# Optimization experiments

Measured on AMD Instinct MI355X. Metric: run time of the kernel, lower is better.

## Reference

```python
import jax, jax.numpy as jnp
import numpy as np

B, C, H, W = 4, 192, 128, 128
NH = 6
HD = C // NH            # 32
GS = 8                  # window (group) size
K = 16                  # unfold kernel size
STRIDE, PAD = 8, 4
NUM = H // GS           # 16 groups per side
BG = B * NUM * NUM      # 1024 windows
N = GS * GS             # 64 tokens per group
KK = K * K              # 256 sampled tokens per window
SCALE = HD ** -0.5


def _rope(x):
    # lucidrains-style rotary embedding along dim -2 (positions), last dim = head_dim
    d = x.shape[-1]
    inv = 1.0 / (10000.0 ** (jnp.arange(0, d, 2, dtype=jnp.float32) / d))
    t = jnp.arange(x.shape[-2], dtype=jnp.float32)
    freqs = jnp.repeat(t[:, None] * inv[None, :], 2, axis=-1)  # [seq, d], interleaved
    cos, sin = jnp.cos(freqs), jnp.sin(freqs)
    xp = x.reshape(x.shape[:-1] + (d // 2, 2))
    xr = jnp.stack((-xp[..., 1], xp[..., 0]), axis=-1).reshape(x.shape)
    return x * cos + xr * sin


def _l2norm(x):
    # torch F.normalize(dim=-1): x / max(||x||, eps)
    n = jnp.linalg.norm(x, axis=-1, keepdims=True)
    return x / jnp.maximum(n, 1e-12)


def setup_inputs() -> dict:
    key = jax.random.key(0)
    ks = jax.random.split(key, 6)
    return {
        "x_complete": jax.random.normal(ks[0], (B, C, H, W), jnp.float32),
        "graph": jax.random.randint(ks[1], (BG, 1, N, KK), 0, 2) > 0,
        "w_group": jax.random.normal(ks[2], (C, C), jnp.float32) * 0.02,
        "b_group": jnp.zeros((C,), jnp.float32),
        "w_sample": jax.random.normal(ks[3], (2 * C, C), jnp.float32) * 0.02,
        "b_sample": jnp.zeros((2 * C,), jnp.float32),
        "w_proj": jax.random.normal(ks[4], (C, C), jnp.float32) * 0.02,
        "b_proj": jnp.zeros((C,), jnp.float32),
    }


def reference(x_complete, graph, w_group, b_group, w_sample, b_sample, w_proj, b_proj):
    # --- local grouping: [B,C,(numh sh),(numw sw)] -> [(B numh numw), sh*sw, C]
    xg = x_complete.reshape(B, C, NUM, GS, NUM, GS).transpose(0, 2, 4, 3, 5, 1).reshape(BG, N, C)
    # --- proj_group: 1x1 Conv1d over channels, then split heads 'b (h c) n -> b h n c'
    x1 = jnp.einsum('bnc,dc->bnd', xg, w_group) + b_group
    x1 = x1.reshape(BG, N, NH, HD).transpose(0, 2, 1, 3)            # [BG,NH,N,HD]
    # --- proj_sample: 1x1 Conv2d to 2C channels
    xs = jnp.einsum('bchw,dc->bdhw', x_complete, w_sample) + b_sample[None, :, None, None]
    # --- F.unfold(kernel=16, stride=8, pad=4): patch features channel-major (c,k0,k1)
    patches = jax.lax.conv_general_dilated_patches(
        xs, (K, K), (STRIDE, STRIDE), ((PAD, PAD), (PAD, PAD)))    # [B, 2C*KK, NUM, NUM]
    xs = patches.reshape(B, 2 * C, KK, NUM * NUM).transpose(0, 3, 2, 1).reshape(BG, KK, 2 * C)
    # --- 'b n (div h c) -> div b h n c'
    xs = xs.reshape(BG, KK, 2, NH, HD)
    x2 = xs[:, :, 0].transpose(0, 2, 1, 3)                          # [BG,NH,KK,HD]
    feat = xs[:, :, 1].transpose(0, 2, 1, 3)                        # [BG,NH,KK,HD]
    # --- RoPE + masked cosine-sim attention
    q = _rope(x1)
    k = _rope(x2)
    sim = jnp.einsum('bhmc,bhnc->bhmn', _l2norm(q), _l2norm(k))
    sim = sim + (-100.0) * (~graph).astype(sim.dtype)
    corr = jax.nn.softmax(sim * SCALE, axis=-1)                     # [BG,NH,N,KK]
    out = jnp.einsum('bhmn,bhnc->bhmc', corr, feat)                 # [BG,NH,N,HD]
    out = out.transpose(0, 2, 1, 3).reshape(BG, N, C)
    return out @ w_proj.T + b_proj
```

## Files before the change

### kernel.cpp

```cpp
#include <hip/hip_runtime.h>
#include <hip/hip_bf16.h>

#define B_    4
#define C_    192
#define C2_   384
#define PIX_  16384
#define NH_   6
#define BG_   1024
#define SCALE_ 0.17677669529663687f
#define C1_ 0.2550348943f

typedef __attribute__((ext_vector_type(8))) short short8v;
typedef __attribute__((ext_vector_type(4))) float f32x4;

__device__ __forceinline__ unsigned cvt_pk_bf16(float lo, float hi) {
    unsigned r;
    asm("v_cvt_pk_bf16_f32 %0, %1, %2" : "=v"(r) : "v"(lo), "v"(hi));
    return r;
}

__global__ __launch_bounds__(256, 1)
void k_rope_init(float2* __restrict__ tbl) {
    int e = blockIdx.x * 256 + threadIdx.x;
    if (e >= 4096) return;
    int pos = e >> 4, j = e & 15;
    float freq = powf(10.0f, -0.25f * (float)j);
    float ang = (float)pos * freq;
    float sn, cs;
    sincosf(ang, &sn, &cs);
    tbl[e] = make_float2(cs, sn);
}

__global__ __launch_bounds__(256, 4)
void k_gmask(const int* __restrict__ g, unsigned int* __restrict__ gbits) {
    int e = blockIdx.x * 256 + threadIdx.x;
    const uint4* p = (const uint4*)(g + (size_t)e * 32);
    unsigned int m = 0u;
#pragma unroll
    for (int i = 0; i < 8; ++i) {
        uint4 v = p[i];
        m |= (v.x ? 1u : 0u) << (i * 4);
        m |= (v.y ? 1u : 0u) << (i * 4 + 1);
        m |= (v.z ? 1u : 0u) << (i * 4 + 2);
        m |= (v.w ? 1u : 0u) << (i * 4 + 3);
    }
    gbits[e] = m;
}

__global__ __launch_bounds__(256, 4)
void k_wcast(const float* __restrict__ wsm, const float* __restrict__ wgb,
             const float* __restrict__ wpj, __hip_bfloat16* __restrict__ wb)
{
    int e = (blockIdx.x * 256 + threadIdx.x) * 4;
    float4 v = (e < 73728) ? *(const float4*)(wsm + e)
             : (e < 110592) ? *(const float4*)(wgb + (e - 73728))
                            : *(const float4*)(wpj + (e - 110592));
    uint2 pk = make_uint2(cvt_pk_bf16(v.x, v.y), cvt_pk_bf16(v.z, v.w));
    *(uint2*)(wb + e) = pk;
}

__global__ __launch_bounds__(256, 4)
void k_convm(const float* __restrict__ x, const __hip_bfloat16* __restrict__ wb,
             const float* __restrict__ bsm, const float* __restrict__ bgb,
             const float2* __restrict__ tbl,
             __hip_bfloat16* __restrict__ xsk, __hip_bfloat16* __restrict__ xsv,
             __hip_bfloat16* __restrict__ qbf)
{
    __shared__ __align__(16) char smem[25600];
    const int bid = blockIdx.x;
    const int b = bid >> 8, pt = bid & 255;
    const int px0 = pt * 64;
    const int t = threadIdx.x;

    {
        const int px = t & 63, cq = t >> 6;
        const float* src = x + ((size_t)b * C_ + cq * 48) * PIX_ + px0 + px;
        char* row = smem + px * 400 + cq * 96;
#pragma unroll
        for (int i = 0; i < 6; ++i) {
            float f[8];
#pragma unroll
            for (int j = 0; j < 8; ++j) f[j] = src[(size_t)(i * 8 + j) * PIX_];
            uint4 pk4;
            pk4.x = cvt_pk_bf16(f[0], f[1]); pk4.y = cvt_pk_bf16(f[2], f[3]);
            pk4.z = cvt_pk_bf16(f[4], f[5]); pk4.w = cvt_pk_bf16(f[6], f[7]);
            *(uint4*)(row + i * 16) = pk4;
        }
    }
    __syncthreads();

    const int w = t >> 6, lane = t & 63;
    const int l15 = lane & 15, g = lane >> 4;
    const int mb = (w & 1) * 32;
    const int nb = (w >> 1) * 32;

    short8v xf0[6], xf1[6];
#pragma unroll
    for (int ks = 0; ks < 6; ++ks) {
        xf0[ks] = *(const short8v*)(smem + (mb + l15) * 400      + ks * 64 + g * 16);
        xf1[ks] = *(const short8v*)(smem + (mb + 16 + l15) * 400 + ks * 64 + g * 16);
    }

    const f32x4 zz = {0.0f, 0.0f, 0.0f, 0.0f};

#pragma unroll
    for (int o2 = 0; o2 < 3; ++o2) {
        const int oct = 3 + o2;
        f32x4 acc00 = zz, acc01 = zz, acc10 = zz, acc11 = zz;
        const __hip_bfloat16* w0 = wb + (size_t)(oct * 64 + nb + l15) * C_;
        const __hip_bfloat16* w1 = w0 + 16 * C_;
#pragma unroll
        for (int ks = 0; ks < 6; ++ks) {
            const short8v b0 = *(const short8v*)(w0 + ks * 32 + g * 8);
            const short8v b1 = *(const short8v*)(w1 + ks * 32 + g * 8);
            acc00 = __builtin_amdgcn_mfma_f32_16x16x32_bf16(xf0[ks], b0, acc00, 0, 0, 0);
            acc01 = __builtin_amdgcn_mfma_f32_16x16x32_bf16(xf0[ks], b1, acc01, 0, 0, 0);
            acc10 = __builtin_amdgcn_mfma_f32_16x16x32_bf16(xf1[ks], b0, acc10, 0, 0, 0);
            acc11 = __builtin_amdgcn_mfma_f32_16x16x32_bf16(xf1[ks], b1, acc11, 0, 0, 0);
        }
        const float bo0 = bsm[oct * 64 + nb + l15];
        const float bo1 = bsm[oct * 64 + nb + 16 + l15];
        uint2 p00 = make_uint2(cvt_pk_bf16(acc00[0] + bo0, acc00[1] + bo0),
                               cvt_pk_bf16(acc00[2] + bo0, acc00[3] + bo0));
        uint2 p10 = make_uint2(cvt_pk_bf16(acc10[0] + bo0, acc10[1] + bo0),
                               cvt_pk_bf16(acc10[2] + bo0, acc10[3] + bo0));
        uint2 p01 = make_uint2(cvt_pk_bf16(acc01[0] + bo1, acc01[1] + bo1),
                               cvt_pk_bf16(acc01[2] + bo1, acc01[3] + bo1));
        uint2 p11 = make_uint2(cvt_pk_bf16(acc11[0] + bo1, acc11[1] + bo1),
                               cvt_pk_bf16(acc11[2] + bo1, acc11[3] + bo1));
        __hip_bfloat16* d0 = xsv + (size_t)(b * C_ + o2 * 64 + nb + l15) * PIX_
                                 + px0 + mb + g * 4;
        *(uint2*)d0        = p00;
        *(uint2*)(d0 + 16) = p10;
        __hip_bfloat16* d1 = d0 + (size_t)16 * PIX_;
        *(uint2*)d1        = p01;
        *(uint2*)(d1 + 16) = p11;
    }

#pragma unroll
    for (int o2 = 0; o2 < 3; ++o2) {
        const int oct = o2;
        f32x4 a00 = zz, a01 = zz, a10 = zz, a11 = zz;
        const __hip_bfloat16* w0 = wb + (size_t)(oct * 64 + nb + l15) * C_;
        const __hip_bfloat16* w1 = w0 + 16 * C_;
#pragma unroll
        for (int ks = 0; ks < 6; ++ks) {
            const short8v wf0 = *(const short8v*)(w0 + ks * 32 + g * 8);
            const short8v wf1 = *(const short8v*)(w1 + ks * 32 + g * 8);
            a00 = __builtin_amdgcn_mfma_f32_16x16x32_bf16(wf0, xf0[ks], a00, 0, 0, 0);
            a01 = __builtin_amdgcn_mfma_f32_16x16x32_bf16(wf0, xf1[ks], a01, 0, 0, 0);
            a10 = __builtin_amdgcn_mfma_f32_16x16x32_bf16(wf1, xf0[ks], a10, 0, 0, 0);
            a11 = __builtin_amdgcn_mfma_f32_16x16x32_bf16(wf1, xf1[ks], a11, 0, 0, 0);
        }
        const float4 bv0 = *(const float4*)(bsm + oct * 64 + nb + g * 4);
        const float4 bv1 = *(const float4*)(bsm + oct * 64 + nb + 16 + g * 4);
        a00[0] += bv0.x; a00[1] += bv0.y; a00[2] += bv0.z; a00[3] += bv0.w;
        a01[0] += bv0.x; a01[1] += bv0.y; a01[2] += bv0.z; a01[3] += bv0.w;
        a10[0] += bv1.x; a10[1] += bv1.y; a10[2] += bv1.z; a10[3] += bv1.w;
        a11[0] += bv1.x; a11[1] += bv1.y; a11[2] += bv1.z; a11[3] += bv1.w;
        float s0 = 0.0f, s1 = 0.0f;
#pragma unroll
        for (int j = 0; j < 4; ++j) {
            s0 = fmaf(a00[j], a00[j], s0); s0 = fmaf(a10[j], a10[j], s0);
            s1 = fmaf(a01[j], a01[j], s1); s1 = fmaf(a11[j], a11[j], s1);
        }
        s0 += __shfl_xor(s0, 16); s0 += __shfl_xor(s0, 32);
        s1 += __shfl_xor(s1, 16); s1 += __shfl_xor(s1, 32);
        const float inv0 = 1.0f / fmaxf(sqrtf(s0), 1e-12f);
        const float inv1 = 1.0f / fmaxf(sqrtf(s1), 1e-12f);
        uint2 q00 = make_uint2(cvt_pk_bf16(a00[0] * inv0, a00[1] * inv0),
                               cvt_pk_bf16(a00[2] * inv0, a00[3] * inv0));
        uint2 q10 = make_uint2(cvt_pk_bf16(a10[0] * inv0, a10[1] * inv0),
                               cvt_pk_bf16(a10[2] * inv0, a10[3] * inv0));
        uint2 q01 = make_uint2(cvt_pk_bf16(a01[0] * inv1, a01[1] * inv1),
                               cvt_pk_bf16(a01[2] * inv1, a01[3] * inv1));
        uint2 q11 = make_uint2(cvt_pk_bf16(a11[0] * inv1, a11[1] * inv1),
                               cvt_pk_bf16(a11[2] * inv1, a11[3] * inv1));
        __hip_bfloat16* d0 = xsk + ((size_t)b * PIX_ + px0 + mb + l15) * C_
                                 + oct * 64 + nb + g * 4;
        *(uint2*)d0        = q00;
        *(uint2*)(d0 + 16) = q10;
        __hip_bfloat16* d1 = d0 + (size_t)16 * C_;
        *(uint2*)d1        = q01;
        *(uint2*)(d1 + 16) = q11;
    }

    const int r = pt >> 1;
    const int c0q = (pt & 1) * 64 + mb + l15;
    const int n0 = (r & 7) * 8 + (c0q & 7);
    const int n1 = (r & 7) * 8 + ((c0q + 16) & 7);
    const int bg0 = (b << 8) + ((r >> 3) << 4) + (c0q >> 3);
    const int bg1 = (b << 8) + ((r >> 3) << 4) + ((c0q + 16) >> 3);
#pragma unroll
    for (int o2 = 0; o2 < 3; ++o2) {
        const int oct = 6 + o2;
        f32x4 a00 = zz, a01 = zz, a10 = zz, a11 = zz;
        const __hip_bfloat16* w0 = wb + (size_t)(oct * 64 + nb + l15) * C_;
        const __hip_bfloat16* w1 = w0 + 16 * C_;
#pragma unroll
        for (int ks = 0; ks < 6; ++ks) {
            const short8v wf0 = *(const short8v*)(w0 + ks * 32 + g * 8);
            const short8v wf1 = *(const short8v*)(w1 + ks * 32 + g * 8);
            a00 = __builtin_amdgcn_mfma_f32_16x16x32_bf16(wf0, xf0[ks], a00, 0, 0, 0);
            a01 = __builtin_amdgcn_mfma_f32_16x16x32_bf16(wf0, xf1[ks], a01, 0, 0, 0);
            a10 = __builtin_amdgcn_mfma_f32_16x16x32_bf16(wf1, xf0[ks], a10, 0, 0, 0);
            a11 = __builtin_amdgcn_mfma_f32_16x16x32_bf16(wf1, xf1[ks], a11, 0, 0, 0);
        }
        const float4 bv0 = *(const float4*)(bgb + (oct - 6) * 64 + nb + g * 4);
        const float4 bv1 = *(const float4*)(bgb + (oct - 6) * 64 + nb + 16 + g * 4);
        a00[0] += bv0.x; a00[1] += bv0.y; a00[2] += bv0.z; a00[3] += bv0.w;
        a01[0] += bv0.x; a01[1] += bv0.y; a01[2] += bv0.z; a01[3] += bv0.w;
        a10[0] += bv1.x; a10[1] += bv1.y; a10[2] += bv1.z; a10[3] += bv1.w;
        a11[0] += bv1.x; a11[1] += bv1.y; a11[2] += bv1.z; a11[3] += bv1.w;
        {
            float2 cA, cB;
            cA = tbl[n0 * 16 + g * 2]; cB = tbl[n0 * 16 + g * 2 + 1];
            { float u0 = a00[0], u1 = a00[1];
              a00[0] = u0 * cA.x - u1 * cA.y; a00[1] = u1 * cA.x + u0 * cA.y; }
            { float u0 = a00[2], u1 = a00[3];
              a00[2] = u0 * cB.x - u1 * cB.y; a00[3] = u1 * cB.x + u0 * cB.y; }
            cA = tbl[n0 * 16 + 8 + g * 2]; cB = tbl[n0 * 16 + 8 + g * 2 + 1];
            { float u0 = a10[0], u1 = a10[1];
              a10[0] = u0 * cA.x - u1 * cA.y; a10[1] = u1 * cA.x + u0 * cA.y; }
            { float u0 = a10[2], u1 = a10[3];
              a10[2] = u0 * cB.x - u1 * cB.y; a10[3] = u1 * cB.x + u0 * cB.y; }
            cA = tbl[n1 * 16 + g * 2]; cB = tbl[n1 * 16 + g * 2 + 1];
            { float u0 = a01[0], u1 = a01[1];
              a01[0] = u0 * cA.x - u1 * cA.y; a01[1] = u1 * cA.x + u0 * cA.y; }
            { float u0 = a01[2], u1 = a01[3];
              a01[2] = u0 * cB.x - u1 * cB.y; a01[3] = u1 * cB.x + u0 * cB.y; }
            cA = tbl[n1 * 16 + 8 + g * 2]; cB = tbl[n1 * 16 + 8 + g * 2 + 1];
            { float u0 = a11[0], u1 = a11[1];
              a11[0] = u0 * cA.x - u1 * cA.y; a11[1] = u1 * cA.x + u0 * cA.y; }
            { float u0 = a11[2], u1 = a11[3];
              a11[2] = u0 * cB.x - u1 * cB.y; a11[3] = u1 * cB.x + u0 * cB.y; }
        }
        float s0 = 0.0f, s1 = 0.0f;
#pragma unroll
        for (int j = 0; j < 4; ++j) {
            s0 = fmaf(a00[j], a00[j], s0); s0 = fmaf(a10[j], a10[j], s0);
            s1 = fmaf(a01[j], a01[j], s1); s1 = fmaf(a11[j], a11[j], s1);
        }
        s0 += __shfl_xor(s0, 16); s0 += __shfl_xor(s0, 32);
        s1 += __shfl_xor(s1, 16); s1 += __shfl_xor(s1, 32);
        const float inv0 = 1.0f / fmaxf(sqrtf(s0), 1e-12f);
        const float inv1 = 1.0f / fmaxf(sqrtf(s1), 1e-12f);
        uint2 q00 = make_uint2(cvt_pk_bf16(a00[0] * inv0, a00[1] * inv0),
                               cvt_pk_bf16(a00[2] * inv0, a00[3] * inv0));
        uint2 q10 = make_uint2(cvt_pk_bf16(a10[0] * inv0, a10[1] * inv0),
                               cvt_pk_bf16(a10[2] * inv0, a10[3] * inv0));
        uint2 q01 = make_uint2(cvt_pk_bf16(a01[0] * inv1, a01[1] * inv1),
                               cvt_pk_bf16(a01[2] * inv1, a01[3] * inv1));
        uint2 q11 = make_uint2(cvt_pk_bf16(a11[0] * inv1, a11[1] * inv1),
                               cvt_pk_bf16(a11[2] * inv1, a11[3] * inv1));
        const int hglob = (oct - 6) * 2 + (nb >> 5);
        __hip_bfloat16* d0 = qbf + (((size_t)bg0 * NH_ + hglob) * 64 + n0) * 32 + g * 4;
        *(uint2*)d0        = q00;
        *(uint2*)(d0 + 16) = q10;
        __hip_bfloat16* d1 = qbf + (((size_t)bg1 * NH_ + hglob) * 64 + n1) * 32 + g * 4;
        *(uint2*)d1        = q01;
        *(uint2*)(d1 + 16) = q11;
    }
}

__global__ __launch_bounds__(512, 2)
void k_attn(const __hip_bfloat16* __restrict__ xsk, const __hip_bfloat16* __restrict__ xsv,
            const unsigned int* __restrict__ gbits, const __hip_bfloat16* __restrict__ qb,
            const float2* __restrict__ tbl, float* __restrict__ attn)
{
    __shared__ __align__(16) char smem[52736];
    const int bid0 = blockIdx.x;
    const int bid = (bid0 & 7) * 768 + (bid0 >> 3);
    const int h = bid % NH_;
    const int bg = bid / NH_;
    const int b = bg >> 8, ph = (bg >> 4) & 15, pw = bg & 15;
    const int t = threadIdx.x;
    const int w = t >> 6, lane = t & 63;
    const int g = lane >> 4, l15 = lane & 15;
    const int rbase = (w & 3) * 16;
    const int wcol  = w >> 2;
    const int cb    = wcol * 128;
    const int cb32  = wcol * 4;

    const short8v qa = *(const short8v*)(qb +
        ((size_t)(bg * NH_ + h) * 64 + rbase + l15) * 32 + g * 8);

    {
        const int m = t >> 1, half = t & 1;
        const int k0 = m >> 4, k1 = m & 15;
        const int rr = ph * 8 - 4 + k0, cc = pw * 8 - 4 + k1;
        const bool inb = ((unsigned)rr < 128u) && ((unsigned)cc < 128u);
        float kv[16];
        if (inb) {
            const uint4* pk = (const uint4*)(xsk +
                ((size_t)b * PIX_ + rr * 128 + cc) * C_ + h * 32 + half * 16);
            union { uint4 u; __hip_bfloat16 h8[8]; } r0, r1;
            r0.u = pk[0]; r1.u = pk[1];
#pragma unroll
            for (int d = 0; d < 8; ++d) {
                kv[d]     = __bfloat162float(r0.h8[d]);
                kv[8 + d] = __bfloat162float(r1.h8[d]);
            }
        } else {
#pragma unroll
            for (int d = 0; d < 16; ++d) kv[d] = 0.0f;
        }
        unsigned pk8[8];
#pragma unroll
        for (int p = 0; p < 8; ++p) {
            float2 cs = tbl[m * 16 + half * 8 + p];
            float a0 = kv[2 * p], a1 = kv[2 * p + 1];
            float e0 = a0 * cs.x - a1 * cs.y;
            float e1 = a1 * cs.x + a0 * cs.y;
            pk8[p] = cvt_pk_bf16(e0, e1);
        }
        *(uint4*)(smem + m * 80 + half * 32)      = make_uint4(pk8[0], pk8[1], pk8[2], pk8[3]);
        *(uint4*)(smem + m * 80 + half * 32 + 16) = make_uint4(pk8[4], pk8[5], pk8[6], pk8[7]);
    }

    {
        const int d = t & 31, k0 = t >> 5;
        const int rr = ph * 8 - 4 + k0;
        const int c0 = pw * 8 - 4;
        char* dst = smem + 34816 + d * 528 + k0 * 32;
        const __hip_bfloat16* src = xsv + (size_t)(b * C_ + h * 32 + d) * PIX_ + rr * 128 + c0;
        const bool rok = (unsigned)rr < 128u;
        if (rok && pw >= 1 && pw <= 14) {
            const uint2* s2 = (const uint2*)src;
            uint2 a0 = s2[0], a1 = s2[1], a2 = s2[2], a3 = s2[3];
            ((uint4*)dst)[0] = make_uint4(a0.x, a0.y, a1.x, a1.y);
            ((uint4*)dst)[1] = make_uint4(a2.x, a2.y, a3.x, a3.y);
        } else {
            __hip_bfloat16* dh = (__hip_bfloat16*)dst;
            __hip_bfloat16 z = __float2bfloat16(0.0f);
#pragma unroll
            for (int i = 0; i < 16; ++i) {
                bool ok = rok && ((unsigned)(c0 + i) < 128u);
                dh[i] = ok ? src[i] : z;
            }
        }
    }

    {
        unsigned int* gbl = (unsigned int*)(smem + 20480);
        const int q = t >> 3, wd = t & 7;
        gbl[q * 9 + wd] = gbits[(size_t)bg * 512 + t];
    }
    __syncthreads();

    f32x4 acc[8];
    const f32x4 zz = {0.0f, 0.0f, 0.0f, 0.0f};
#pragma unroll
    for (int tile = 0; tile < 8; ++tile) {
        const short8v kb = *(const short8v*)(smem + (cb + tile * 16 + l15) * 80 + g * 16);
        acc[tile] = __builtin_amdgcn_mfma_f32_16x16x32_bf16(kb, qa, zz, 0, 0, 0);
    }

    const unsigned int* gbl = (const unsigned int*)(smem + 20480);
    float* reds = (float*)(smem + 51712);
    {
        const int q = rbase + l15;
        const unsigned int wv[4] = { gbl[q * 9 + cb32], gbl[q * 9 + cb32 + 1],
                                     gbl[q * 9 + cb32 + 2], gbl[q * 9 + cb32 + 3] };
        float sm = 0.0f;
#pragma unroll
        for (int tile = 0; tile < 8; ++tile) {
            const unsigned int bits = wv[tile >> 1] >> ((tile & 1) * 16 + (g << 2));
#pragma unroll
            for (int j = 0; j < 4; ++j) {
                float e = __builtin_amdgcn_exp2f(fmaf(acc[tile][j], C1_, -C1_));
                e = ((bits >> j) & 1u) ? e : 0.0f;
                acc[tile][j] = e;
                sm += e;
            }
        }
        sm += __shfl_xor(sm, 16);
        sm += __shfl_xor(sm, 32);
        if (lane < 16) reds[q * 2 + wcol] = sm;
    }
    __syncthreads();

    float inv4[4];
#pragma unroll
    for (int j = 0; j < 4; ++j) {
        const int qq = rbase + (g << 2) + j;
        float2 rr2 = *(const float2*)&reds[qq * 2];
        inv4[j] = 1.0f / (rr2.x + rr2.y + 1e-37f);
    }

    char* plw = smem + w * 4352;
#pragma unroll
    for (int tile = 0; tile < 8; ++tile) {
        uint2 pw2 = make_uint2(cvt_pk_bf16(acc[tile][0], acc[tile][1]),
                               cvt_pk_bf16(acc[tile][2], acc[tile][3]));
        *(uint2*)(plw + l15 * 272 + tile * 32 + g * 8) = pw2;
    }

    f32x4 o0 = zz, o1 = zz;
#pragma unroll
    for (int ks = 0; ks < 4; ++ks) {
        const short8v pa  = *(const short8v*)(plw + l15 * 272 + (ks * 32 + g * 8) * 2);
        const short8v vb0 = *(const short8v*)(smem + 34816 + l15 * 528        + (cb + ks * 32 + g * 8) * 2);
        const short8v vb1 = *(const short8v*)(smem + 34816 + (16 + l15) * 528 + (cb + ks * 32 + g * 8) * 2);
        o0 = __builtin_amdgcn_mfma_f32_16x16x32_bf16(pa, vb0, o0, 0, 0, 0);
        o1 = __builtin_amdgcn_mfma_f32_16x16x32_bf16(pa, vb1, o1, 0, 0, 0);
    }
    __syncthreads();

    float* ob = (float*)smem;
    if (wcol == 1) {
#pragma unroll
        for (int j = 0; j < 4; ++j) {
            const int q = rbase + g * 4 + j;
            ob[q * 33 + l15]      = o0[j];
            ob[q * 33 + 16 + l15] = o1[j];
        }
    }
    __syncthreads();
    if (wcol == 0) {
#pragma unroll
        for (int j = 0; j < 4; ++j) {
            const int q = rbase + g * 4 + j;
            float v0 = (o0[j] + ob[q * 33 + l15])      * inv4[j];
            float v1 = (o1[j] + ob[q * 33 + 16 + l15]) * inv4[j];
            attn[((size_t)bg * 64 + q) * 192 + h * 32 + l15]      = v0;
            attn[((size_t)bg * 64 + q) * 192 + h * 32 + 16 + l15] = v1;
        }
    }
}

__global__ __launch_bounds__(256, 4)
void k_oprojm(const float* __restrict__ attn, const __hip_bfloat16* __restrict__ wpb,
              const float* __restrict__ bp, float* __restrict__ out)
{
    __shared__ __align__(16) char smem[25600];
    const int bid0 = blockIdx.x;
    const int bid = (bid0 & 7) * 384 + (bid0 >> 3);
    const int oct = bid % 3;
    const int rt  = bid / 3;
    const int row0 = rt * 64;
    const int t = threadIdx.x;

#pragma unroll
    for (int e0 = 0; e0 < 12; ++e0) {
        const int e = e0 * 256 + t;
        const int r = e / 48, c4 = e % 48;
        float4 v = *(const float4*)(attn + (size_t)(row0 + r) * 192 + c4 * 4);
        uint2 pk = make_uint2(cvt_pk_bf16(v.x, v.y), cvt_pk_bf16(v.z, v.w));
        *(uint2*)(smem + r * 400 + c4 * 8) = pk;
    }
    __syncthreads();

    const int w = t >> 6, lane = t & 63;
    const int l15 = lane & 15, g = lane >> 4;
    const int mb = (w & 1) * 32;
    const int nb = (w >> 1) * 32;

    const f32x4 zz = {0.0f, 0.0f, 0.0f, 0.0f};
    f32x4 acc00 = zz, acc01 = zz, acc10 = zz, acc11 = zz;
    const __hip_bfloat16* w0 = wpb + (size_t)(oct * 64 + nb + l15) * C_;
    const __hip_bfloat16* w1 = w0 + 16 * C_;
#pragma unroll
    for (int ks = 0; ks < 6; ++ks) {
        const short8v a0 = *(const short8v*)(smem + (mb + l15) * 400      + ks * 64 + g * 16);
        const short8v a1 = *(const short8v*)(smem + (mb + 16 + l15) * 400 + ks * 64 + g * 16);
        const short8v b0 = *(const short8v*)(w0 + ks * 32 + g * 8);
        const short8v b1 = *(const short8v*)(w1 + ks * 32 + g * 8);
        acc00 = __builtin_amdgcn_mfma_f32_16x16x32_bf16(a0, b0, acc00, 0, 0, 0);
        acc01 = __builtin_amdgcn_mfma_f32_16x16x32_bf16(a0, b1, acc01, 0, 0, 0);
        acc10 = __builtin_amdgcn_mfma_f32_16x16x32_bf16(a1, b0, acc10, 0, 0, 0);
        acc11 = __builtin_amdgcn_mfma_f32_16x16x32_bf16(a1, b1, acc11, 0, 0, 0);
    }
    __syncthreads();

    float* ot = (float*)smem;
#pragma unroll
    for (int j = 0; j < 4; ++j) {
        ot[(mb + g * 4 + j) * 68      + nb + l15]      = acc00[j];
        ot[(mb + 16 + g * 4 + j) * 68 + nb + l15]      = acc10[j];
        ot[(mb + g * 4 + j) * 68      + nb + 16 + l15] = acc01[j];
        ot[(mb + 16 + g * 4 + j) * 68 + nb + 16 + l15] = acc11[j];
    }
    __syncthreads();

    {
        const int k = t & 15, pxi = t >> 4;
        const float4 bias4 = *(const float4*)(bp + oct * 64 + k * 4);
#pragma unroll
        for (int p = 0; p < 4; ++p) {
            const int px = p * 16 + pxi;
            float4 v = *(const float4*)&ot[px * 68 + k * 4];
            v.x += bias4.x; v.y += bias4.y; v.z += bias4.z; v.w += bias4.w;
            *(float4*)(out + (size_t)(row0 + px) * 192 + oct * 64 + k * 4) = v;
        }
    }
}

extern "C" void kernel_launch(void* const* d_in, const int* in_sizes, int n_in,
                              void* d_out, int out_size, void* d_ws, size_t ws_size,
                              hipStream_t stream)
{
    (void)in_sizes; (void)n_in; (void)out_size; (void)ws_size;
    const float* x   = (const float*)d_in[0];
    const int* grph  = (const int*)d_in[1];
    const float* wg  = (const float*)d_in[2];
    const float* bgb = (const float*)d_in[3];
    const float* wsm = (const float*)d_in[4];
    const float* bsm = (const float*)d_in[5];
    const float* wp  = (const float*)d_in[6];
    const float* bp  = (const float*)d_in[7];
    float* out = (float*)d_out;

    char* wsb = (char*)d_ws;
    __hip_bfloat16* xsk = (__hip_bfloat16*)wsb;
    __hip_bfloat16* xsv = (__hip_bfloat16*)(wsb + 25165824ull);
    __hip_bfloat16* qbf = (__hip_bfloat16*)(wsb + 50331648ull);
    float2* tbl = (float2*)(wsb + 75497472ull);
    unsigned int* gbits = (unsigned int*)(wsb + 75530240ull);
    __hip_bfloat16* wb  = (__hip_bfloat16*)(wsb + 77627392ull);
    __hip_bfloat16* wpb = wb + 110592;

    hipLaunchKernelGGL(k_rope_init, dim3(16),   dim3(256), 0, stream, tbl);
    hipLaunchKernelGGL(k_wcast,     dim3(144),  dim3(256), 0, stream, wsm, wg, wp, wb);
    hipLaunchKernelGGL(k_gmask,     dim3(2048), dim3(256), 0, stream, grph, gbits);
    hipLaunchKernelGGL(k_convm,     dim3(1024), dim3(256), 0, stream, x, wb, bsm, bgb, tbl, xsk, xsv, qbf);
    hipLaunchKernelGGL(k_attn,      dim3(6144), dim3(512), 0, stream, xsk, xsv, gbits, qbf, tbl, out);
    hipLaunchKernelGGL(k_oprojm,    dim3(3072), dim3(256), 0, stream, out, wpb, bp, out);
}
```

Before: 186.0 us.

## Halve k_convm pixel tile to 32 and double grid with XCD-aware block swizzle

The fused 1x1-conv kernel now processes 32 pixels per block instead of 64, so each wave computes a 16x32 output tile with half the accumulators and A-fragments. Shared memory per block halves, launch bounds request 8 blocks/SM, and the grid doubles to 2048 blocks. Block indices are remapped so consecutive hardware blocks land on the same XCD. This aims for more occupancy and better latency hiding, at the cost of reloading weight fragments twice as often per pixel.

```diff
diff --git a/kernel.cpp b/kernel.cpp
--- a/kernel.cpp
+++ b/kernel.cpp
@@ -59,25 +59,26 @@
     *(uint2*)(wb + e) = pk;
 }
 
-__global__ __launch_bounds__(256, 4)
+__global__ __launch_bounds__(256, 8)
 void k_convm(const float* __restrict__ x, const __hip_bfloat16* __restrict__ wb,
              const float* __restrict__ bsm, const float* __restrict__ bgb,
              const float2* __restrict__ tbl,
              __hip_bfloat16* __restrict__ xsk, __hip_bfloat16* __restrict__ xsv,
              __hip_bfloat16* __restrict__ qbf)
 {
-    __shared__ __align__(16) char smem[25600];
-    const int bid = blockIdx.x;
-    const int b = bid >> 8, pt = bid & 255;
-    const int px0 = pt * 64;
+    __shared__ __align__(16) char smem[12800];
+    const int bid0 = blockIdx.x;
+    const int bid = (bid0 & 7) * 256 + (bid0 >> 3);
+    const int b = bid >> 9, pt = bid & 511;
+    const int px0 = pt * 32;
     const int t = threadIdx.x;
 
     {
-        const int px = t & 63, cq = t >> 6;
-        const float* src = x + ((size_t)b * C_ + cq * 48) * PIX_ + px0 + px;
-        char* row = smem + px * 400 + cq * 96;
-#pragma unroll
-        for (int i = 0; i < 6; ++i) {
+        const int px = t & 31, cq = t >> 5;
+        const float* src = x + ((size_t)b * C_ + cq * 24) * PIX_ + px0 + px;
+        char* row = smem + px * 400 + cq * 48;
+#pragma unroll
+        for (int i = 0; i < 3; ++i) {
             float f[8];
 #pragma unroll
             for (int j = 0; j < 8; ++j) f[j] = src[(size_t)(i * 8 + j) * PIX_];
@@ -91,175 +92,125 @@
 
     const int w = t >> 6, lane = t & 63;
     const int l15 = lane & 15, g = lane >> 4;
-    const int mb = (w & 1) * 32;
-    const int nb = (w >> 1) * 32;
-
-    short8v xf0[6], xf1[6];
-#pragma unroll
-    for (int ks = 0; ks < 6; ++ks) {
-        xf0[ks] = *(const short8v*)(smem + (mb + l15) * 400      + ks * 64 + g * 16);
-        xf1[ks] = *(const short8v*)(smem + (mb + 16 + l15) * 400 + ks * 64 + g * 16);
-    }
+    const int pb2 = (w & 1) * 16;
+    const int ob2 = (w >> 1) * 32;
+
+    short8v xf[6];
+#pragma unroll
+    for (int ks = 0; ks < 6; ++ks)
+        xf[ks] = *(const short8v*)(smem + (pb2 + l15) * 400 + ks * 64 + g * 16);
 
     const f32x4 zz = {0.0f, 0.0f, 0.0f, 0.0f};
 
 #pragma unroll
     for (int o2 = 0; o2 < 3; ++o2) {
         const int oct = 3 + o2;
-        f32x4 acc00 = zz, acc01 = zz, acc10 = zz, acc11 = zz;
-        const __hip_bfloat16* w0 = wb + (size_t)(oct * 64 + nb + l15) * C_;
+        f32x4 acc0 = zz, acc1 = zz;
+        const __hip_bfloat16* w0 = wb + (size_t)(oct * 64 + ob2 + l15) * C_;
         const __hip_bfloat16* w1 = w0 + 16 * C_;
 #pragma unroll
         for (int ks = 0; ks < 6; ++ks) {
             const short8v b0 = *(const short8v*)(w0 + ks * 32 + g * 8);
             const short8v b1 = *(const short8v*)(w1 + ks * 32 + g * 8);
-            acc00 = __builtin_amdgcn_mfma_f32_16x16x32_bf16(xf0[ks], b0, acc00, 0, 0, 0);
-            acc01 = __builtin_amdgcn_mfma_f32_16x16x32_bf16(xf0[ks], b1, acc01, 0, 0, 0);
-            acc10 = __builtin_amdgcn_mfma_f32_16x16x32_bf16(xf1[ks], b0, acc10, 0, 0, 0);
-            acc11 = __builtin_amdgcn_mfma_f32_16x16x32_bf16(xf1[ks], b1, acc11, 0, 0, 0);
-        }
-        const float bo0 = bsm[oct * 64 + nb + l15];
-        const float bo1 = bsm[oct * 64 + nb + 16 + l15];
-        uint2 p00 = make_uint2(cvt_pk_bf16(acc00[0] + bo0, acc00[1] + bo0),
-                               cvt_pk_bf16(acc00[2] + bo0, acc00[3] + bo0));
-        uint2 p10 = make_uint2(cvt_pk_bf16(acc10[0] + bo0, acc10[1] + bo0),
-                               cvt_pk_bf16(acc10[2] + bo0, acc10[3] + bo0));
-        uint2 p01 = make_uint2(cvt_pk_bf16(acc01[0] + bo1, acc01[1] + bo1),
-                               cvt_pk_bf16(acc01[2] + bo1, acc01[3] + bo1));
-        uint2 p11 = make_uint2(cvt_pk_bf16(acc11[0] + bo1, acc11[1] + bo1),
-                               cvt_pk_bf16(acc11[2] + bo1, acc11[3] + bo1));
-        __hip_bfloat16* d0 = xsv + (size_t)(b * C_ + o2 * 64 + nb + l15) * PIX_
-                                 + px0 + mb + g * 4;
-        *(uint2*)d0        = p00;
-        *(uint2*)(d0 + 16) = p10;
-        __hip_bfloat16* d1 = d0 + (size_t)16 * PIX_;
-        *(uint2*)d1        = p01;
-        *(uint2*)(d1 + 16) = p11;
+            acc0 = __builtin_amdgcn_mfma_f32_16x16x32_bf16(xf[ks], b0, acc0, 0, 0, 0);
+            acc1 = __builtin_amdgcn_mfma_f32_16x16x32_bf16(xf[ks], b1, acc1, 0, 0, 0);
+        }
+        const float bo0 = bsm[oct * 64 + ob2 + l15];
+        const float bo1 = bsm[oct * 64 + ob2 + 16 + l15];
+        uint2 p0 = make_uint2(cvt_pk_bf16(acc0[0] + bo0, acc0[1] + bo0),
+                              cvt_pk_bf16(acc0[2] + bo0, acc0[3] + bo0));
+        uint2 p1 = make_uint2(cvt_pk_bf16(acc1[0] + bo1, acc1[1] + bo1),
+                              cvt_pk_bf16(acc1[2] + bo1, acc1[3] + bo1));
+        __hip_bfloat16* d0 = xsv + (size_t)(b * C_ + o2 * 64 + ob2 + l15) * PIX_
+                                 + px0 + pb2 + g * 4;
+        *(uint2*)d0 = p0;
+        *(uint2*)(d0 + (size_t)16 * PIX_) = p1;
     }
 
 #pragma unroll
     for (int o2 = 0; o2 < 3; ++o2) {
         const int oct = o2;
-        f32x4 a00 = zz, a01 = zz, a10 = zz, a11 = zz;
-        const __hip_bfloat16* w0 = wb + (size_t)(oct * 64 + nb + l15) * C_;
+        f32x4 a0 = zz, a1 = zz;
+        const __hip_bfloat16* w0 = wb + (size_t)(oct * 64 + ob2 + l15) * C_;
         const __hip_bfloat16* w1 = w0 + 16 * C_;
 #pragma unroll
         for (int ks = 0; ks < 6; ++ks) {
             const short8v wf0 = *(const short8v*)(w0 + ks * 32 + g * 8);
             const short8v wf1 = *(const short8v*)(w1 + ks * 32 + g * 8);
-            a00 = __builtin_amdgcn_mfma_f32_16x16x32_bf16(wf0, xf0[ks], a00, 0, 0, 0);
-            a01 = __builtin_amdgcn_mfma_f32_16x16x32_bf16(wf0, xf1[ks], a01, 0, 0, 0);
-            a10 = __builtin_amdgcn_mfma_f32_16x16x32_bf16(wf1, xf0[ks], a10, 0, 0, 0);
-            a11 = __builtin_amdgcn_mfma_f32_16x16x32_bf16(wf1, xf1[ks], a11, 0, 0, 0);
-        }
-        const float4 bv0 = *(const float4*)(bsm + oct * 64 + nb + g * 4);
-        const float4 bv1 = *(const float4*)(bsm + oct * 64 + nb + 16 + g * 4);
-        a00[0] += bv0.x; a00[1] += bv0.y; a00[2] += bv0.z; a00[3] += bv0.w;
-        a01[0] += bv0.x; a01[1] += bv0.y; a01[2] += bv0.z; a01[3] += bv0.w;
-        a10[0] += bv1.x; a10[1] += bv1.y; a10[2] += bv1.z; a10[3] += bv1.w;
-        a11[0] += bv1.x; a11[1] += bv1.y; a11[2] += bv1.z; a11[3] += bv1.w;
-        float s0 = 0.0f, s1 = 0.0f;
+            a0 = __builtin_amdgcn_mfma_f32_16x16x32_bf16(wf0, xf[ks], a0, 0, 0, 0);
+            a1 = __builtin_amdgcn_mfma_f32_16x16x32_bf16(wf1, xf[ks], a1, 0, 0, 0);
+        }
+        const float4 bv0 = *(const float4*)(bsm + oct * 64 + ob2 + g * 4);
+        const float4 bv1 = *(const float4*)(bsm + oct * 64 + ob2 + 16 + g * 4);
+        a0[0] += bv0.x; a0[1] += bv0.y; a0[2] += bv0.z; a0[3] += bv0.w;
+        a1[0] += bv1.x; a1[1] += bv1.y; a1[2] += bv1.z; a1[3] += bv1.w;
+        float s = 0.0f;
 #pragma unroll
         for (int j = 0; j < 4; ++j) {
-            s0 = fmaf(a00[j], a00[j], s0); s0 = fmaf(a10[j], a10[j], s0);
-            s1 = fmaf(a01[j], a01[j], s1); s1 = fmaf(a11[j], a11[j], s1);
-        }
-        s0 += __shfl_xor(s0, 16); s0 += __shfl_xor(s0, 32);
-        s1 += __shfl_xor(s1, 16); s1 += __shfl_xor(s1, 32);
-        const float inv0 = 1.0f / fmaxf(sqrtf(s0), 1e-12f);
-        const float inv1 = 1.0f / fmaxf(sqrtf(s1), 1e-12f);
-        uint2 q00 = make_uint2(cvt_pk_bf16(a00[0] * inv0, a00[1] * inv0),
-                               cvt_pk_bf16(a00[2] * inv0, a00[3] * inv0));
-        uint2 q10 = make_uint2(cvt_pk_bf16(a10[0] * inv0, a10[1] * inv0),
-                               cvt_pk_bf16(a10[2] * inv0, a10[3] * inv0));
-        uint2 q01 = make_uint2(cvt_pk_bf16(a01[0] * inv1, a01[1] * inv1),
-                               cvt_pk_bf16(a01[2] * inv1, a01[3] * inv1));
-        uint2 q11 = make_uint2(cvt_pk_bf16(a11[0] * inv1, a11[1] * inv1),
-                               cvt_pk_bf16(a11[2] * inv1, a11[3] * inv1));
-        __hip_bfloat16* d0 = xsk + ((size_t)b * PIX_ + px0 + mb + l15) * C_
-                                 + oct * 64 + nb + g * 4;
-        *(uint2*)d0        = q00;
-        *(uint2*)(d0 + 16) = q10;
-        __hip_bfloat16* d1 = d0 + (size_t)16 * C_;
-        *(uint2*)d1        = q01;
-        *(uint2*)(d1 + 16) = q11;
-    }
-
-    const int r = pt >> 1;
-    const int c0q = (pt & 1) * 64 + mb + l15;
-    const int n0 = (r & 7) * 8 + (c0q & 7);
-    const int n1 = (r & 7) * 8 + ((c0q + 16) & 7);
-    const int bg0 = (b << 8) + ((r >> 3) << 4) + (c0q >> 3);
-    const int bg1 = (b << 8) + ((r >> 3) << 4) + ((c0q + 16) >> 3);
+            s = fmaf(a0[j], a0[j], s);
+            s = fmaf(a1[j], a1[j], s);
+        }
+        s += __shfl_xor(s, 16); s += __shfl_xor(s, 32);
+        const float inv = 1.0f / fmaxf(sqrtf(s), 1e-12f);
+        uint2 q0 = make_uint2(cvt_pk_bf16(a0[0] * inv, a0[1] * inv),
+                              cvt_pk_bf16(a0[2] * inv, a0[3] * inv));
+        uint2 q1 = make_uint2(cvt_pk_bf16(a1[0] * inv, a1[1] * inv),
+                              cvt_pk_bf16(a1[2] * inv, a1[3] * inv));
+        __hip_bfloat16* d = xsk + ((size_t)b * PIX_ + px0 + pb2 + l15) * C_
+                                + oct * 64 + ob2 + g * 4;
+        *(uint2*)d        = q0;
+        *(uint2*)(d + 16) = q1;
+    }
+
+    const int p  = px0 + pb2 + l15;
+    const int r  = p >> 7, c = p & 127;
+    const int n  = (r & 7) * 8 + (c & 7);
+    const int bg = (b << 8) + ((r >> 3) << 4) + (c >> 3);
 #pragma unroll
     for (int o2 = 0; o2 < 3; ++o2) {
         const int oct = 6 + o2;
-        f32x4 a00 = zz, a01 = zz, a10 = zz, a11 = zz;
-        const __hip_bfloat16* w0 = wb + (size_t)(oct * 64 + nb + l15) * C_;
+        f32x4 a0 = zz, a1 = zz;
+        const __hip_bfloat16* w0 = wb + (size_t)(oct * 64 + ob2 + l15) * C_;
         const __hip_bfloat16* w1 = w0 + 16 * C_;
 #pragma unroll
         for (int ks = 0; ks < 6; ++ks) {
             const short8v wf0 = *(const short8v*)(w0 + ks * 32 + g * 8);
             const short8v wf1 = *(const short8v*)(w1 + ks * 32 + g * 8);
-            a00 = __builtin_amdgcn_mfma_f32_16x16x32_bf16(wf0, xf0[ks], a00, 0, 0, 0);
-            a01 = __builtin_amdgcn_mfma_f32_16x16x32_bf16(wf0, xf1[ks], a01, 0, 0, 0);
-            a10 = __builtin_amdgcn_mfma_f32_16x16x32_bf16(wf1, xf0[ks], a10, 0, 0, 0);
-            a11 = __builtin_amdgcn_mfma_f32_16x16x32_bf16(wf1, xf1[ks], a11, 0, 0, 0);
-        }
-        const float4 bv0 = *(const float4*)(bgb + (oct - 6) * 64 + nb + g * 4);
-        const float4 bv1 = *(const float4*)(bgb + (oct - 6) * 64 + nb + 16 + g * 4);
-        a00[0] += bv0.x; a00[1] += bv0.y; a00[2] += bv0.z; a00[3] += bv0.w;
-        a01[0] += bv0.x; a01[1] += bv0.y; a01[2] += bv0.z; a01[3] += bv0.w;
-        a10[0] += bv1.x; a10[1] += bv1.y; a10[2] += bv1.z; a10[3] += bv1.w;
-        a11[0] += bv1.x; a11[1] += bv1.y; a11[2] += bv1.z; a11[3] += bv1.w;
+            a0 = __builtin_amdgcn_mfma_f32_16x16x32_bf16(wf0, xf[ks], a0, 0, 0, 0);
+            a1 = __builtin_amdgcn_mfma_f32_16x16x32_bf16(wf1, xf[ks], a1, 0, 0, 0);
+        }
+        const float4 bv0 = *(const float4*)(bgb + (oct - 6) * 64 + ob2 + g * 4);
+        const float4 bv1 = *(const float4*)(bgb + (oct - 6) * 64 + ob2 + 16 + g * 4);
+        a0[0] += bv0.x; a0[1] += bv0.y; a0[2] += bv0.z; a0[3] += bv0.w;
+        a1[0] += bv1.x; a1[1] += bv1.y; a1[2] += bv1.z; a1[3] += bv1.w;
         {
-            float2 cA, cB;
-            cA = tbl[n0 * 16 + g * 2]; cB = tbl[n0 * 16 + g * 2 + 1];
-            { float u0 = a00[0], u1 = a00[1];
-              a00[0] = u0 * cA.x - u1 * cA.y; a00[1] = u1 * cA.x + u0 * cA.y; }
-            { float u0 = a00[2], u1 = a00[3];
-              a00[2] = u0 * cB.x - u1 * cB.y; a00[3] = u1 * cB.x + u0 * cB.y; }
-            cA = tbl[n0 * 16 + 8 + g * 2]; cB = tbl[n0 * 16 + 8 + g * 2 + 1];
-            { float u0 = a10[0], u1 = a10[1];
-              a10[0] = u0 * cA.x - u1 * cA.y; a10[1] = u1 * cA.x + u0 * cA.y; }
-            { float u0 = a10[2], u1 = a10[3];
-              a10[2] = u0 * cB.x - u1 * cB.y; a10[3] = u1 * cB.x + u0 * cB.y; }
-            cA = tbl[n1 * 16 + g * 2]; cB = tbl[n1 * 16 + g * 2 + 1];
-            { float u0 = a01[0], u1 = a01[1];
-              a01[0] = u0 * cA.x - u1 * cA.y; a01[1] = u1 * cA.x + u0 * cA.y; }
-            { float u0 = a01[2], u1 = a01[3];
-              a01[2] = u0 * cB.x - u1 * cB.y; a01[3] = u1 * cB.x + u0 * cB.y; }
-            cA = tbl[n1 * 16 + 8 + g * 2]; cB = tbl[n1 * 16 + 8 + g * 2 + 1];
-            { float u0 = a11[0], u1 = a11[1];
-              a11[0] = u0 * cA.x - u1 * cA.y; a11[1] = u1 * cA.x + u0 * cA.y; }
-            { float u0 = a11[2], u1 = a11[3];
-              a11[2] = u0 * cB.x - u1 * cB.y; a11[3] = u1 * cB.x + u0 * cB.y; }
-        }
-        float s0 = 0.0f, s1 = 0.0f;
+            float2 cA = tbl[n * 16 + 2 * g], cB = tbl[n * 16 + 2 * g + 1];
+            { float u0 = a0[0], u1 = a0[1];
+              a0[0] = u0 * cA.x - u1 * cA.y; a0[1] = u1 * cA.x + u0 * cA.y; }
+            { float u0 = a0[2], u1 = a0[3];
+              a0[2] = u0 * cB.x - u1 * cB.y; a0[3] = u1 * cB.x + u0 * cB.y; }
+            cA = tbl[n * 16 + 8 + 2 * g]; cB = tbl[n * 16 + 8 + 2 * g + 1];
+            { float u0 = a1[0], u1 = a1[1];
+              a1[0] = u0 * cA.x - u1 * cA.y; a1[1] = u1 * cA.x + u0 * cA.y; }
+            { float u0 = a1[2], u1 = a1[3];
+              a1[2] = u0 * cB.x - u1 * cB.y; a1[3] = u1 * cB.x + u0 * cB.y; }
+        }
+        float s = 0.0f;
 #pragma unroll
         for (int j = 0; j < 4; ++j) {
-            s0 = fmaf(a00[j], a00[j], s0); s0 = fmaf(a10[j], a10[j], s0);
-            s1 = fmaf(a01[j], a01[j], s1); s1 = fmaf(a11[j], a11[j], s1);
-        }
-        s0 += __shfl_xor(s0, 16); s0 += __shfl_xor(s0, 32);
-        s1 += __shfl_xor(s1, 16); s1 += __shfl_xor(s1, 32);
-        const float inv0 = 1.0f / fmaxf(sqrtf(s0), 1e-12f);
-        const float inv1 = 1.0f / fmaxf(sqrtf(s1), 1e-12f);
-        uint2 q00 = make_uint2(cvt_pk_bf16(a00[0] * inv0, a00[1] * inv0),
-                               cvt_pk_bf16(a00[2] * inv0, a00[3] * inv0));
-        uint2 q10 = make_uint2(cvt_pk_bf16(a10[0] * inv0, a10[1] * inv0),
-                               cvt_pk_bf16(a10[2] * inv0, a10[3] * inv0));
-        uint2 q01 = make_uint2(cvt_pk_bf16(a01[0] * inv1, a01[1] * inv1),
-                               cvt_pk_bf16(a01[2] * inv1, a01[3] * inv1));
-        uint2 q11 = make_uint2(cvt_pk_bf16(a11[0] * inv1, a11[1] * inv1),
-                               cvt_pk_bf16(a11[2] * inv1, a11[3] * inv1));
-        const int hglob = (oct - 6) * 2 + (nb >> 5);
-        __hip_bfloat16* d0 = qbf + (((size_t)bg0 * NH_ + hglob) * 64 + n0) * 32 + g * 4;
-        *(uint2*)d0        = q00;
-        *(uint2*)(d0 + 16) = q10;
-        __hip_bfloat16* d1 = qbf + (((size_t)bg1 * NH_ + hglob) * 64 + n1) * 32 + g * 4;
-        *(uint2*)d1        = q01;
-        *(uint2*)(d1 + 16) = q11;
+            s = fmaf(a0[j], a0[j], s);
+            s = fmaf(a1[j], a1[j], s);
+        }
+        s += __shfl_xor(s, 16); s += __shfl_xor(s, 32);
+        const float inv = 1.0f / fmaxf(sqrtf(s), 1e-12f);
+        uint2 q0 = make_uint2(cvt_pk_bf16(a0[0] * inv, a0[1] * inv),
+                              cvt_pk_bf16(a0[2] * inv, a0[3] * inv));
+        uint2 q1 = make_uint2(cvt_pk_bf16(a1[0] * inv, a1[1] * inv),
+                              cvt_pk_bf16(a1[2] * inv, a1[3] * inv));
+        const int hglob = (oct - 6) * 2 + (ob2 >> 5);
+        __hip_bfloat16* d = qbf + (((size_t)bg * NH_ + hglob) * 64 + n) * 32 + g * 4;
+        *(uint2*)d        = q0;
+        *(uint2*)(d + 16) = q1;
     }
 }
 
@@ -523,7 +474,7 @@
     hipLaunchKernelGGL(k_rope_init, dim3(16),   dim3(256), 0, stream, tbl);
     hipLaunchKernelGGL(k_wcast,     dim3(144),  dim3(256), 0, stream, wsm, wg, wp, wb);
     hipLaunchKernelGGL(k_gmask,     dim3(2048), dim3(256), 0, stream, grph, gbits);
-    hipLaunchKernelGGL(k_convm,     dim3(1024), dim3(256), 0, stream, x, wb, bsm, bgb, tbl, xsk, xsv, qbf);
+    hipLaunchKernelGGL(k_convm,     dim3(2048), dim3(256), 0, stream, x, wb, bsm, bgb, tbl, xsk, xsv, qbf);
     hipLaunchKernelGGL(k_attn,      dim3(6144), dim3(512), 0, stream, xsk, xsv, gbits, qbf, tbl, out);
     hipLaunchKernelGGL(k_oprojm,    dim3(3072), dim3(256), 0, stream, out, wpb, bp, out);
 }
```

New measurement: 240.1 us. 29.1% more time.
